# Optimization experiments

Hardware: AMD Instinct MI355X
Metric: run time of the kernel (lower is better)

## Reference

```python
import jax, jax.numpy as jnp
import numpy as np

HIDDEN = 256
HORIZON = 24
FMET = 16
OUT = 1
EPS = 1e-5


def setup_inputs() -> dict:
    key = jax.random.key(0)
    ks = jax.random.split(key, 12)
    B, N = 16, 1000
    final_h = jax.random.normal(ks[0], (B, N, HIDDEN), dtype=jnp.float32)
    future_met = jax.random.normal(ks[1], (B, HORIZON, N, FMET), dtype=jnp.float32)
    # step_queries: xavier_uniform over (max_horizon, hidden)
    lim_q = float(np.sqrt(6.0 / (HORIZON + HIDDEN)))
    step_queries = jax.random.uniform(ks[2], (HORIZON, HIDDEN), minval=-lim_q, maxval=lim_q, dtype=jnp.float32)
    # future_met_proj: Linear(FMET -> HIDDEN); store weight as (FMET, HIDDEN)
    lim_fm = float(np.sqrt(1.0 / FMET))
    W_fm = jax.random.uniform(ks[3], (FMET, HIDDEN), minval=-lim_fm, maxval=lim_fm, dtype=jnp.float32)
    b_fm = jax.random.uniform(ks[4], (HIDDEN,), minval=-lim_fm, maxval=lim_fm, dtype=jnp.float32)
    gamma = jnp.ones((HIDDEN,), dtype=jnp.float32)
    beta = jnp.zeros((HIDDEN,), dtype=jnp.float32)
    lim1 = float(np.sqrt(1.0 / HIDDEN))
    W1 = jax.random.uniform(ks[5], (HIDDEN, HIDDEN), minval=-lim1, maxval=lim1, dtype=jnp.float32)
    b1 = jax.random.uniform(ks[6], (HIDDEN,), minval=-lim1, maxval=lim1, dtype=jnp.float32)
    W2 = jax.random.uniform(ks[7], (HIDDEN, OUT), minval=-lim1, maxval=lim1, dtype=jnp.float32)
    b2 = jax.random.uniform(ks[8], (OUT,), minval=-lim1, maxval=lim1, dtype=jnp.float32)
    return {
        "final_h": final_h,
        "future_met": future_met,
        "step_queries": step_queries,
        "W_fm": W_fm,
        "b_fm": b_fm,
        "gamma": gamma,
        "beta": beta,
        "W1": W1,
        "b1": b1,
        "W2": W2,
        "b2": b2,
    }


def _layer_norm(x, gamma, beta):
    mu = jnp.mean(x, axis=-1, keepdims=True)
    var = jnp.mean(jnp.square(x - mu), axis=-1, keepdims=True)
    return (x - mu) * jax.lax.rsqrt(var + EPS) * gamma + beta


def reference(final_h, future_met, step_queries, W_fm, b_fm, gamma, beta, W1, b1, W2, b2):
    # final_h: (B, N, H); future_met: (B, T, N, F)
    # combined: (B, N, T, H) = broadcast(final_h) + queries + proj(future_met)
    combined = final_h[:, :, None, :] + step_queries[None, None, :, :]
    fm = jnp.transpose(future_met, (0, 2, 1, 3))  # (B, N, T, F)
    combined = combined + (jnp.einsum("bntf,fh->bnth", fm, W_fm) + b_fm)
    x = _layer_norm(combined, gamma, beta)
    x = jax.nn.gelu(x @ W1 + b1, approximate=False)
    # dropout is identity in eval mode
    out = x @ W2 + b2  # (B, N, T, OUT)
    return jnp.transpose(out, (0, 2, 1, 3))  # (B, T, N, OUT)
```

## Files before the change

kernel.cpp:

```cpp
#include <hip/hip_runtime.h>
#include <hip/hip_bf16.h>
#include <stdint.h>

#define MROWS 32
#define LDA   264
#define FMS   40

typedef __bf16 bf16x8 __attribute__((ext_vector_type(8)));
typedef float  f32x4  __attribute__((ext_vector_type(4)));
typedef float  f32x2  __attribute__((ext_vector_type(2)));

__device__ __forceinline__ unsigned short f2bf(float f) {
    union { float f; uint32_t u; } v; v.f = f;
    return (unsigned short)((v.u + 0x7FFFu + ((v.u >> 16) & 1u)) >> 16);
}

__device__ __forceinline__ ushort2 pk_bf16(float a, float b) {
    union { __hip_bfloat162 v; ushort2 u; } c;
    c.v = __float22bfloat162_rn(make_float2(a, b));
    return c.u;
}

template <int CTRL>
__device__ __forceinline__ float dpp_radd(float x) {
    union { float f; int i; } a, b;
    a.f = x;
    b.i = __builtin_amdgcn_update_dpp(0, a.i, CTRL, 0xF, 0xF, true);
    return x + b.f;
}
#define ROW_SHR1 0x111
#define ROW_SHR2 0x112
#define ROW_SHR4 0x114
#define ROW_SHR8 0x118
__device__ __forceinline__ float dpp_rowsum(float x) {
    x = dpp_radd<ROW_SHR1>(x);
    x = dpp_radd<ROW_SHR2>(x);
    x = dpp_radd<ROW_SHR4>(x);
    x = dpp_radd<ROW_SHR8>(x);
    return x;
}

__device__ __forceinline__ f32x2 gelu_fast2(f32x2 v) {
    const f32x2 t = v * v;
    f32x2 p = t * 0.044715f + 1.0f;
    const f32x2 u = v * p;
    f32x2 e;
    e.x = __builtin_amdgcn_exp2f(u.x * -2.3021131160186336f);
    e.y = __builtin_amdgcn_exp2f(u.y * -2.3021131160186336f);
    f32x2 r;
    r.x = __builtin_amdgcn_rcpf(1.0f + e.x);
    r.y = __builtin_amdgcn_rcpf(1.0f + e.y);
    return v * r;
}

__device__ __forceinline__ int frag_n(int f) {
    return (f & 0xC0) | ((f & 3) << 4) | ((f >> 2) & 15);
}

__global__ __launch_bounds__(256) void prep1(const float* __restrict__ W1,
                                             const float* __restrict__ step_q,
                                             const float* __restrict__ b_fm,
                                             const float* __restrict__ W_fm,
                                             const float* __restrict__ gamma,
                                             const float* __restrict__ beta,
                                             unsigned short* __restrict__ w1frag,
                                             float* __restrict__ sqb,
                                             unsigned short* __restrict__ wfmfrag,
                                             float* __restrict__ gpart,
                                             float* __restrict__ bpart) {
    const int blk = blockIdx.x, tid = threadIdx.x;
    if (blk < 8) {
        __shared__ unsigned short T[256][40];
        const int kk = blk;
        float sg = 0.f, sb = 0.f;
        #pragma unroll
        for (int r = 0; r < 32; ++r) {
            const int klog = frag_n((kk << 5) + r);
            const float wv = W1[klog * 256 + tid];
            const float gv = gamma[klog];
            sg = fmaf(gv, wv, sg);
            sb = fmaf(beta[klog], wv, sb);
            T[tid][r] = f2bf(wv * gv);
        }
        gpart[(kk << 8) + tid] = sg;
        bpart[(kk << 8) + tid] = sb;
        __syncthreads();
        #pragma unroll
        for (int f = 0; f < 4; ++f) {
            const int fi = (f << 8) + tid;
            const int l = fi & 63, j = (fi >> 6) & 3, w = fi >> 8;
            const int n = (w << 6) + (j << 4) + (l & 15);
            const uint4 v = *(const uint4*)&T[n][(l >> 4) << 3];
            *(uint4*)&w1frag[((w << 5) + (j << 3) + kk) * 512 + (l << 3)] = v;
        }
    } else if (blk < 32) {
        const int t = blk - 8;
        const int n = frag_n(tid);
        sqb[t * 256 + tid] = step_q[t * 256 + n] + b_fm[n];
    } else {
        const int f  = blk - 32;
        const int fr = (f << 8) + tid;
        const int l = fr & 63, j = (fr >> 6) & 3, w = fr >> 8;
        const int n = (w << 6) + (j << 4) + (l & 15);
        const int qr = l >> 4;
        #pragma unroll
        for (int e = 0; e < 8; ++e) {
            const int k = (qr << 3) + e;
            wfmfrag[(fr << 3) + e] = (k < 16) ? f2bf(W_fm[(k << 8) + n]) : (unsigned short)0;
        }
    }
}

__global__ __launch_bounds__(256) void prep2(const float* __restrict__ gpart,
                                             const float* __restrict__ bpart,
                                             const float* __restrict__ b1,
                                             const float* __restrict__ W2,
                                             float* __restrict__ gw1f,
                                             float* __restrict__ b1tf,
                                             float* __restrict__ w2f) {
    const int tid = threadIdx.x;
    const int n = frag_n(tid);
    float sg = 0.f, sb = 0.f;
    #pragma unroll
    for (int kk = 0; kk < 8; ++kk) {
        sg += gpart[(kk << 8) + n];
        sb += bpart[(kk << 8) + n];
    }
    gw1f[tid] = sg;
    b1tf[tid] = sb + b1[n];
    w2f[tid]  = W2[n];
}

__global__ __launch_bounds__(256, 6) void fused_head(
    const float* __restrict__ final_h, const float* __restrict__ future_met,
    const float* __restrict__ b2,      const unsigned short* __restrict__ w1frag,
    const float* __restrict__ sqb,     const unsigned short* __restrict__ wfmfrag,
    const float* __restrict__ gw1f,    const float* __restrict__ b1tf,
    const float* __restrict__ w2f,     float* __restrict__ out)
{
    __shared__ __align__(16) unsigned short Abuf[MROWS * LDA];
    __shared__ __align__(16) unsigned short fmA[MROWS * FMS];
    __shared__ float2 red[4][MROWS];
    __shared__ float2 mv[MROWS];
    __shared__ float  part[4][MROWS];

    const int tid = threadIdx.x;
    const int w   = tid >> 6;
    const int l   = tid & 63;
    const int col = l & 15;
    const int qr  = l >> 4;
    const int m0  = blockIdx.x * MROWS;
    const int bn0 = m0 / 24;
    const int tt0 = m0 - bn0 * 24;
    const int fb  = (w << 6) + (col << 2);

    if (tid < 128) {
        const int row = tid >> 2, f0 = (tid & 3) << 2;
        const int tta = tt0 + row;
        const int sub = (tta >= 24) + (tta >= 48);
        const int tt  = tta - sub * 24;
        const int bn  = bn0 + sub;
        const int b   = bn / 1000, n = bn - b * 1000;
        const float4 v = *(const float4*)&future_met[((((b * 24 + tt) * 1000) + n) << 4) + f0];
        ushort2 lo = pk_bf16(v.x, v.y), hi = pk_bf16(v.z, v.w);
        ushort4 o; o.x = lo.x; o.y = lo.y; o.z = hi.x; o.w = hi.y;
        *(ushort4*)&fmA[row * FMS + f0] = o;
    }
    {
        const int row = tid >> 3, k = 16 + ((tid & 7) << 1);
        *(unsigned int*)&fmA[row * FMS + k] = 0u;
    }
    __syncthreads();

    const int dlo = qr << 2;
    const int slo = ((tt0 + dlo) >= 24) + ((tt0 + dlo) >= 48);
    const int shi = ((tt0 + dlo + 19) >= 24) + ((tt0 + dlo + 19) >= 48);
    float flo[4], fhi[4];
    {
        const float* fhl = final_h + ((bn0 + slo) << 8) + (w << 6) + col;
        const float* fhh = final_h + ((bn0 + shi) << 8) + (w << 6) + col;
        #pragma unroll
        for (int j = 0; j < 4; ++j) { flo[j] = fhl[j << 4]; fhi[j] = fhh[j << 4]; }
    }

    f32x4 acc[2][4];
    #pragma unroll
    for (int i = 0; i < 2; ++i) {
        #pragma unroll
        for (int r = 0; r < 4; ++r) {
            const int d   = (i << 4) + (qr << 2) + r;
            const int tta = tt0 + d;
            const int sub = (tta >= 24) + (tta >= 48);
            const int tt  = tta - sub * 24;
            const bool lo = (sub == slo);
            const float4 sb4 = *(const float4*)&sqb[(tt << 8) + fb];
            acc[i][0][r] = (lo ? flo[0] : fhi[0]) + sb4.x;
            acc[i][1][r] = (lo ? flo[1] : fhi[1]) + sb4.y;
            acc[i][2][r] = (lo ? flo[2] : fhi[2]) + sb4.z;
            acc[i][3][r] = (lo ? flo[3] : fhi[3]) + sb4.w;
        }
    }
    {
        const bf16x8 af0 = *(const bf16x8*)&fmA[col * FMS + (qr << 3)];
        const bf16x8 af1 = *(const bf16x8*)&fmA[(16 + col) * FMS + (qr << 3)];
        const unsigned short* Bwf = wfmfrag + (w << 11) + (l << 3);
        #pragma unroll
        for (int j = 0; j < 4; ++j) {
            const bf16x8 bf = *(const bf16x8*)(Bwf + (j << 9));
            acc[0][j] = __builtin_amdgcn_mfma_f32_16x16x32_bf16(af0, bf, acc[0][j], 0, 0, 0);
            acc[1][j] = __builtin_amdgcn_mfma_f32_16x16x32_bf16(af1, bf, acc[1][j], 0, 0, 0);
        }
    }

    #pragma unroll
    for (int i = 0; i < 2; ++i) {
        #pragma unroll
        for (int r = 0; r < 4; ++r) {
            const int m = (i << 4) + (qr << 2) + r;
            const f32x2 vA = {acc[i][0][r], acc[i][1][r]};
            const f32x2 vB = {acc[i][2][r], acc[i][3][r]};
            const f32x2 sv = vA + vB;
            const f32x2 qv = vA * vA + vB * vB;
            float s = sv.x + sv.y;
            float q = qv.x + qv.y;
            const ushort2 p01 = pk_bf16(vA.x, vA.y);
            const ushort2 p23 = pk_bf16(vB.x, vB.y);
            s = dpp_rowsum(s);
            q = dpp_rowsum(q);
            if (col == 15) red[w][m] = make_float2(s, q);
            ushort4 o; o.x = p01.x; o.y = p01.y; o.z = p23.x; o.w = p23.y;
            *(ushort4*)&Abuf[m * LDA + (w << 6) + (col << 2)] = o;
        }
    }
    __syncthreads();

    if (tid < MROWS) {
        const float2 a0 = red[0][tid], a1 = red[1][tid], a2 = red[2][tid], a3 = red[3][tid];
        const float S = a0.x + a1.x + a2.x + a3.x;
        const float Q = a0.y + a1.y + a2.y + a3.y;
        const float mu = S * 0.00390625f;
        const float rstd = rsqrtf(Q * 0.00390625f - mu * mu + 1e-5f);
        mv[tid] = make_float2(mu, rstd);
    }

    #pragma unroll
    for (int i = 0; i < 2; ++i)
        #pragma unroll
        for (int j = 0; j < 4; ++j)
            acc[i][j] = (f32x4){0.f, 0.f, 0.f, 0.f};

    {
        const unsigned short* Bw  = w1frag + (w << 14) + (l << 3);
        const unsigned short* Ab0 = &Abuf[col * LDA + (qr << 3)];
        const unsigned short* Ab1 = &Abuf[(16 + col) * LDA + (qr << 3)];
        #pragma unroll
        for (int kk = 0; kk < 8; ++kk) {
            const bf16x8 a0 = *(const bf16x8*)(Ab0 + (kk << 5));
            const bf16x8 a1 = *(const bf16x8*)(Ab1 + (kk << 5));
            #pragma unroll
            for (int j = 0; j < 4; ++j) {
                const bf16x8 bf = *(const bf16x8*)(Bw + (j << 12) + (kk << 9));
                acc[0][j] = __builtin_amdgcn_mfma_f32_16x16x32_bf16(a0, bf, acc[0][j], 0, 0, 0);
                acc[1][j] = __builtin_amdgcn_mfma_f32_16x16x32_bf16(a1, bf, acc[1][j], 0, 0, 0);
            }
        }
    }

    const float4 gw4 = *(const float4*)&gw1f[fb];
    const float4 bt4 = *(const float4*)&b1tf[fb];
    const float4 w24 = *(const float4*)&w2f[fb];
    const f32x2 gwA = {gw4.x, gw4.y}, gwB = {gw4.z, gw4.w};
    const f32x2 btA = {bt4.x, bt4.y}, btB = {bt4.z, bt4.w};
    const f32x2 w2A = {w24.x, w24.y}, w2B = {w24.z, w24.w};
    __syncthreads();

    #pragma unroll
    for (int i = 0; i < 2; ++i) {
        #pragma unroll
        for (int r = 0; r < 4; ++r) {
            const int m = (i << 4) + (qr << 2) + r;
            const float2 p = mv[m];
            const float cm = -p.x * p.y;
            const f32x2 baseA = gwA * cm + btA;
            const f32x2 baseB = gwB * cm + btB;
            const f32x2 accA = {acc[i][0][r], acc[i][1][r]};
            const f32x2 accB = {acc[i][2][r], acc[i][3][r]};
            const f32x2 yA = accA * p.y + baseA;
            const f32x2 yB = accB * p.y + baseB;
            const f32x2 gvA = gelu_fast2(yA);
            const f32x2 gvB = gelu_fast2(yB);
            const f32x2 pp2 = gvA * w2A + gvB * w2B;
            float pp = pp2.x + pp2.y;
            pp = dpp_rowsum(pp);
            if (col == 15) part[w][m] = pp;
        }
    }
    __syncthreads();

    if (tid < MROWS) {
        const int m = m0 + tid;
        const float val = part[0][tid] + part[1][tid] + part[2][tid] + part[3][tid] + b2[0];
        const int bn = m / 24, tt = m - bn * 24;
        const int b  = bn / 1000, n = bn - b * 1000;
        out[(b * 24 + tt) * 1000 + n] = val;
    }
}

extern "C" void kernel_launch(void* const* d_in, const int* in_sizes, int n_in,
                              void* d_out, int out_size, void* d_ws, size_t ws_size,
                              hipStream_t stream) {
    const float* final_h    = (const float*)d_in[0];
    const float* future_met = (const float*)d_in[1];
    const float* step_q     = (const float*)d_in[2];
    const float* W_fm       = (const float*)d_in[3];
    const float* b_fm       = (const float*)d_in[4];
    const float* gamma      = (const float*)d_in[5];
    const float* beta       = (const float*)d_in[6];
    const float* W1         = (const float*)d_in[7];
    const float* b1         = (const float*)d_in[8];
    const float* W2         = (const float*)d_in[9];
    const float* b2         = (const float*)d_in[10];

    unsigned short* w1frag  = (unsigned short*)d_ws;
    float*          sqb     = (float*)((char*)d_ws + 131072);
    unsigned short* wfmfrag = (unsigned short*)((char*)d_ws + 155648);
    float*          gpart   = (float*)((char*)d_ws + 188416);
    float*          bpart   = (float*)((char*)d_ws + 196608);
    float*          gw1f    = (float*)((char*)d_ws + 204800);
    float*          b1tf    = (float*)((char*)d_ws + 205824);
    float*          w2f     = (float*)((char*)d_ws + 206848);
    float* out = (float*)d_out;

    prep1<<<36, 256, 0, stream>>>(W1, step_q, b_fm, W_fm, gamma, beta,
                                  w1frag, sqb, wfmfrag, gpart, bpart);
    prep2<<<1, 256, 0, stream>>>(gpart, bpart, b1, W2, gw1f, b1tf, w2f);
    fused_head<<<12000, 256, 0, stream>>>(final_h, future_met, b2,
                                          w1frag, sqb, wfmfrag, gw1f, b1tf, w2f, out);
}
```

Before: 199.4 us.

## Distribute W1 over the sum: precompute final_h@W1 per node, small per-step GEMMs

Uses linearity of the first matmul over the input sum (final_h + query + projected met). final_h·(γ∘W1) is computed once per (b,n) in a new prep kernel and stored to workspace. The step-query and met-projection terms are folded into W1 (a 16x256 fragment and a 24x256 table), so the main kernel runs one small K=32 MFMA instead of the full 256x256 GEMM per row. LayerNorm statistics still come from the un-normalized combined vector. This cuts main-kernel matmul work 24-fold at the cost of a 16MB fp32 intermediate write and read, plus a fallback path when workspace is too small.

```diff
diff --git a/kernel.cpp b/kernel.cpp
--- a/kernel.cpp
+++ b/kernel.cpp
@@ -67,10 +67,13 @@
                                              float* __restrict__ sqb,
                                              unsigned short* __restrict__ wfmfrag,
                                              float* __restrict__ gpart,
-                                             float* __restrict__ bpart) {
+                                             float* __restrict__ bpart,
+                                             float* __restrict__ WFWp,
+                                             float* __restrict__ SQWp) {
+    __shared__ unsigned short T[256][40];
+    __shared__ float redw[8][32][41];
     const int blk = blockIdx.x, tid = threadIdx.x;
     if (blk < 8) {
-        __shared__ unsigned short T[256][40];
         const int kk = blk;
         float sg = 0.f, sb = 0.f;
         #pragma unroll
@@ -97,7 +100,7 @@
         const int t = blk - 8;
         const int n = frag_n(tid);
         sqb[t * 256 + tid] = step_q[t * 256 + n] + b_fm[n];
-    } else {
+    } else if (blk < 36) {
         const int f  = blk - 32;
         const int fr = (f << 8) + tid;
         const int l = fr & 63, j = (fr >> 6) & 3, w = fr >> 8;
@@ -107,6 +110,40 @@
         for (int e = 0; e < 8; ++e) {
             const int k = (qr << 3) + e;
             wfmfrag[(fr << 3) + e] = (k < 16) ? f2bf(W_fm[(k << 8) + n]) : (unsigned short)0;
+        }
+    } else {
+        const int kc = tid >> 5, cl = tid & 31;
+        const int n  = ((blk - 36) << 5) + cl;
+        float wfw[16];
+        float sqw[24];
+        #pragma unroll
+        for (int f = 0; f < 16; ++f) wfw[f] = 0.f;
+        #pragma unroll
+        for (int t = 0; t < 24; ++t) sqw[t] = 0.f;
+        for (int hh = 0; hh < 32; ++hh) {
+            const int h = (kc << 5) + hh;
+            const float g1 = gamma[h] * W1[(h << 8) + n];
+            #pragma unroll
+            for (int f = 0; f < 16; ++f)
+                wfw[f] = fmaf(W_fm[(f << 8) + h], g1, wfw[f]);
+            const float bf = b_fm[h];
+            #pragma unroll
+            for (int t = 0; t < 24; ++t)
+                sqw[t] = fmaf(step_q[(t << 8) + h] + bf, g1, sqw[t]);
+        }
+        #pragma unroll
+        for (int f = 0; f < 16; ++f) redw[kc][cl][f] = wfw[f];
+        #pragma unroll
+        for (int t = 0; t < 24; ++t) redw[kc][cl][16 + t] = sqw[t];
+        __syncthreads();
+        for (int e = tid; e < 1280; e += 256) {
+            const int cl2 = e & 31, v = e >> 5;
+            float s = 0.f;
+            #pragma unroll
+            for (int k2 = 0; k2 < 8; ++k2) s += redw[k2][cl2][v];
+            const int nn = ((blk - 36) << 5) + cl2;
+            if (v < 16) WFWp[(v << 8) + nn] = s;
+            else        SQWp[((v - 16) << 8) + nn] = s;
         }
     }
 }
@@ -131,14 +168,111 @@
     w2f[tid]  = W2[n];
 }
 
+__global__ __launch_bounds__(256) void prep3(const float* __restrict__ final_h,
+                                             const unsigned short* __restrict__ w1frag,
+                                             const float* __restrict__ gpart,
+                                             const float* __restrict__ bpart,
+                                             const float* __restrict__ b1,
+                                             const float* __restrict__ W2,
+                                             const float* __restrict__ WFWp,
+                                             const float* __restrict__ SQWp,
+                                             float* __restrict__ gw1f,
+                                             float* __restrict__ b1tf,
+                                             float* __restrict__ w2f,
+                                             unsigned short* __restrict__ wfwfrag,
+                                             float* __restrict__ sqwf,
+                                             float* __restrict__ FHW) {
+    __shared__ __align__(16) unsigned short Abuf[MROWS * LDA];
+    const int blk = blockIdx.x, tid = threadIdx.x;
+    if (blk == 500) {
+        const int n = frag_n(tid);
+        float sg = 0.f, sb = 0.f;
+        #pragma unroll
+        for (int kk = 0; kk < 8; ++kk) {
+            sg += gpart[(kk << 8) + n];
+            sb += bpart[(kk << 8) + n];
+        }
+        gw1f[tid] = sg;
+        b1tf[tid] = sb + b1[n];
+        w2f[tid]  = W2[n];
+        #pragma unroll
+        for (int f = 0; f < 4; ++f) {
+            const int fr = (f << 8) + tid;
+            const int l = fr & 63, j = (fr >> 6) & 3, wq = fr >> 8;
+            const int nn = (wq << 6) + (j << 4) + (l & 15);
+            const int qr2 = l >> 4;
+            #pragma unroll
+            for (int e = 0; e < 8; ++e) {
+                const int k = (qr2 << 3) + e;
+                wfwfrag[(fr << 3) + e] = (k < 16) ? f2bf(WFWp[(k << 8) + nn]) : (unsigned short)0;
+            }
+        }
+        #pragma unroll
+        for (int t = 0; t < 24; ++t)
+            sqwf[(t << 8) + tid] = SQWp[(t << 8) + n];
+        return;
+    }
+    const int w = tid >> 6, l = tid & 63;
+    const int col = l & 15, qr = l >> 4;
+    const int fb = (w << 6) + (col << 2);
+    const int R0 = blk << 5;
+    #pragma unroll
+    for (int i = 0; i < 2; ++i) {
+        #pragma unroll
+        for (int r = 0; r < 4; ++r) {
+            const int m = (i << 4) + (qr << 2) + r;
+            const float* src = final_h + ((R0 + m) << 8) + (w << 6) + col;
+            const ushort2 p01 = pk_bf16(src[0],  src[16]);
+            const ushort2 p23 = pk_bf16(src[32], src[48]);
+            ushort4 o; o.x = p01.x; o.y = p01.y; o.z = p23.x; o.w = p23.y;
+            *(ushort4*)&Abuf[m * LDA + fb] = o;
+        }
+    }
+    __syncthreads();
+    f32x4 acc[2][4];
+    #pragma unroll
+    for (int i = 0; i < 2; ++i)
+        #pragma unroll
+        for (int j = 0; j < 4; ++j)
+            acc[i][j] = (f32x4){0.f, 0.f, 0.f, 0.f};
+    {
+        const unsigned short* Bw  = w1frag + (w << 14) + (l << 3);
+        const unsigned short* Ab0 = &Abuf[col * LDA + (qr << 3)];
+        const unsigned short* Ab1 = &Abuf[(16 + col) * LDA + (qr << 3)];
+        #pragma unroll
+        for (int kk = 0; kk < 8; ++kk) {
+            const bf16x8 a0 = *(const bf16x8*)(Ab0 + (kk << 5));
+            const bf16x8 a1 = *(const bf16x8*)(Ab1 + (kk << 5));
+            #pragma unroll
+            for (int j = 0; j < 4; ++j) {
+                const bf16x8 bf = *(const bf16x8*)(Bw + (j << 12) + (kk << 9));
+                acc[0][j] = __builtin_amdgcn_mfma_f32_16x16x32_bf16(a0, bf, acc[0][j], 0, 0, 0);
+                acc[1][j] = __builtin_amdgcn_mfma_f32_16x16x32_bf16(a1, bf, acc[1][j], 0, 0, 0);
+            }
+        }
+    }
+    #pragma unroll
+    for (int i = 0; i < 2; ++i) {
+        #pragma unroll
+        for (int r = 0; r < 4; ++r) {
+            const int m = (i << 4) + (qr << 2) + r;
+            float4 st;
+            st.x = acc[i][0][r]; st.y = acc[i][1][r];
+            st.z = acc[i][2][r]; st.w = acc[i][3][r];
+            *(float4*)&FHW[((R0 + m) << 8) + fb] = st;
+        }
+    }
+}
+
 __global__ __launch_bounds__(256, 6) void fused_head(
     const float* __restrict__ final_h, const float* __restrict__ future_met,
-    const float* __restrict__ b2,      const unsigned short* __restrict__ w1frag,
-    const float* __restrict__ sqb,     const unsigned short* __restrict__ wfmfrag,
+    const float* __restrict__ b2,      const float* __restrict__ sqb,
+    const unsigned short* __restrict__ wfmfrag,
     const float* __restrict__ gw1f,    const float* __restrict__ b1tf,
-    const float* __restrict__ w2f,     float* __restrict__ out)
+    const float* __restrict__ w2f,     const unsigned short* __restrict__ wfwfrag,
+    const float* __restrict__ sqwf,    const float* __restrict__ FHW,
+    float* __restrict__ out)
 {
-    __shared__ __align__(16) unsigned short Abuf[MROWS * LDA];
     __shared__ __align__(16) unsigned short fmA[MROWS * FMS];
     __shared__ float2 red[4][MROWS];
     __shared__ float2 mv[MROWS];
@@ -200,9 +334,9 @@
             acc[i][3][r] = (lo ? flo[3] : fhi[3]) + sb4.w;
         }
     }
-    {
-        const bf16x8 af0 = *(const bf16x8*)&fmA[col * FMS + (qr << 3)];
-        const bf16x8 af1 = *(const bf16x8*)&fmA[(16 + col) * FMS + (qr << 3)];
+    const bf16x8 af0 = *(const bf16x8*)&fmA[col * FMS + (qr << 3)];
+    const bf16x8 af1 = *(const bf16x8*)&fmA[(16 + col) * FMS + (qr << 3)];
+    {
         const unsigned short* Bwf = wfmfrag + (w << 11) + (l << 3);
         #pragma unroll
         for (int j = 0; j < 4; ++j) {
@@ -223,13 +357,9 @@
             const f32x2 qv = vA * vA + vB * vB;
             float s = sv.x + sv.y;
             float q = qv.x + qv.y;
-            const ushort2 p01 = pk_bf16(vA.x, vA.y);
-            const ushort2 p23 = pk_bf16(vB.x, vB.y);
             s = dpp_rowsum(s);
             q = dpp_rowsum(q);
             if (col == 15) red[w][m] = make_float2(s, q);
-            ushort4 o; o.x = p01.x; o.y = p01.y; o.z = p23.x; o.w = p23.y;
-            *(ushort4*)&Abuf[m * LDA + (w << 6) + (col << 2)] = o;
         }
     }
     __syncthreads();
@@ -244,25 +374,28 @@
     }
 
     #pragma unroll
-    for (int i = 0; i < 2; ++i)
-        #pragma unroll
-        for (int j = 0; j < 4; ++j)
-            acc[i][j] = (f32x4){0.f, 0.f, 0.f, 0.f};
-
-    {
-        const unsigned short* Bw  = w1frag + (w << 14) + (l << 3);
-        const unsigned short* Ab0 = &Abuf[col * LDA + (qr << 3)];
-        const unsigned short* Ab1 = &Abuf[(16 + col) * LDA + (qr << 3)];
-        #pragma unroll
-        for (int kk = 0; kk < 8; ++kk) {
-            const bf16x8 a0 = *(const bf16x8*)(Ab0 + (kk << 5));
-            const bf16x8 a1 = *(const bf16x8*)(Ab1 + (kk << 5));
-            #pragma unroll
-            for (int j = 0; j < 4; ++j) {
-                const bf16x8 bf = *(const bf16x8*)(Bw + (j << 12) + (kk << 9));
-                acc[0][j] = __builtin_amdgcn_mfma_f32_16x16x32_bf16(a0, bf, acc[0][j], 0, 0, 0);
-                acc[1][j] = __builtin_amdgcn_mfma_f32_16x16x32_bf16(a1, bf, acc[1][j], 0, 0, 0);
-            }
+    for (int i = 0; i < 2; ++i) {
+        #pragma unroll
+        for (int r = 0; r < 4; ++r) {
+            const int d   = (i << 4) + (qr << 2) + r;
+            const int tta = tt0 + d;
+            const int sub = (tta >= 24) + (tta >= 48);
+            const int tt  = tta - sub * 24;
+            const float4 fw = *(const float4*)&FHW[((bn0 + sub) << 8) + fb];
+            const float4 sw = *(const float4*)&sqwf[(tt << 8) + fb];
+            acc[i][0][r] = fw.x + sw.x;
+            acc[i][1][r] = fw.y + sw.y;
+            acc[i][2][r] = fw.z + sw.z;
+            acc[i][3][r] = fw.w + sw.w;
+        }
+    }
+    {
+        const unsigned short* Bw2 = wfwfrag + (w << 11) + (l << 3);
+        #pragma unroll
+        for (int j = 0; j < 4; ++j) {
+            const bf16x8 bfv = *(const bf16x8*)(Bw2 + (j << 9));
+            acc[0][j] = __builtin_amdgcn_mfma_f32_16x16x32_bf16(af0, bfv, acc[0][j], 0, 0, 0);
+            acc[1][j] = __builtin_amdgcn_mfma_f32_16x16x32_bf16(af1, bfv, acc[1][j], 0, 0, 0);
         }
     }
 
@@ -306,6 +439,181 @@
     }
 }
 
+__global__ __launch_bounds__(256, 6) void fused_head_v3(
+    const float* __restrict__ final_h, const float* __restrict__ future_met,
+    const float* __restrict__ b2,      const unsigned short* __restrict__ w1frag,
+    const float* __restrict__ sqb,     const unsigned short* __restrict__ wfmfrag,
+    const float* __restrict__ gw1f,    const float* __restrict__ b1tf,
+    const float* __restrict__ w2f,     float* __restrict__ out)
+{
+    __shared__ __align__(16) unsigned short Abuf[MROWS * LDA];
+    __shared__ __align__(16) unsigned short fmA[MROWS * FMS];
+    __shared__ float2 red[4][MROWS];
+    __shared__ float2 mv[MROWS];
+    __shared__ float  part[4][MROWS];
+
+    const int tid = threadIdx.x;
+    const int w   = tid >> 6;
+    const int l   = tid & 63;
+    const int col = l & 15;
+    const int qr  = l >> 4;
+    const int m0  = blockIdx.x * MROWS;
+    const int bn0 = m0 / 24;
+    const int tt0 = m0 - bn0 * 24;
+    const int fb  = (w << 6) + (col << 2);
+
+    if (tid < 128) {
+        const int row = tid >> 2, f0 = (tid & 3) << 2;
+        const int tta = tt0 + row;
+        const int sub = (tta >= 24) + (tta >= 48);
+        const int tt  = tta - sub * 24;
+        const int bn  = bn0 + sub;
+        const int b   = bn / 1000, n = bn - b * 1000;
+        const float4 v = *(const float4*)&future_met[((((b * 24 + tt) * 1000) + n) << 4) + f0];
+        ushort2 lo = pk_bf16(v.x, v.y), hi = pk_bf16(v.z, v.w);
+        ushort4 o; o.x = lo.x; o.y = lo.y; o.z = hi.x; o.w = hi.y;
+        *(ushort4*)&fmA[row * FMS + f0] = o;
+    }
+    {
+        const int row = tid >> 3, k = 16 + ((tid & 7) << 1);
+        *(unsigned int*)&fmA[row * FMS + k] = 0u;
+    }
+    __syncthreads();
+
+    const int dlo = qr << 2;
+    const int slo = ((tt0 + dlo) >= 24) + ((tt0 + dlo) >= 48);
+    const int shi = ((tt0 + dlo + 19) >= 24) + ((tt0 + dlo + 19) >= 48);
+    float flo[4], fhi[4];
+    {
+        const float* fhl = final_h + ((bn0 + slo) << 8) + (w << 6) + col;
+        const float* fhh = final_h + ((bn0 + shi) << 8) + (w << 6) + col;
+        #pragma unroll
+        for (int j = 0; j < 4; ++j) { flo[j] = fhl[j << 4]; fhi[j] = fhh[j << 4]; }
+    }
+
+    f32x4 acc[2][4];
+    #pragma unroll
+    for (int i = 0; i < 2; ++i) {
+        #pragma unroll
+        for (int r = 0; r < 4; ++r) {
+            const int d   = (i << 4) + (qr << 2) + r;
+            const int tta = tt0 + d;
+            const int sub = (tta >= 24) + (tta >= 48);
+            const int tt  = tta - sub * 24;
+            const bool lo = (sub == slo);
+            const float4 sb4 = *(const float4*)&sqb[(tt << 8) + fb];
+            acc[i][0][r] = (lo ? flo[0] : fhi[0]) + sb4.x;
+            acc[i][1][r] = (lo ? flo[1] : fhi[1]) + sb4.y;
+            acc[i][2][r] = (lo ? flo[2] : fhi[2]) + sb4.z;
+            acc[i][3][r] = (lo ? flo[3] : fhi[3]) + sb4.w;
+        }
+    }
+    {
+        const bf16x8 af0 = *(const bf16x8*)&fmA[col * FMS + (qr << 3)];
+        const bf16x8 af1 = *(const bf16x8*)&fmA[(16 + col) * FMS + (qr << 3)];
+        const unsigned short* Bwf = wfmfrag + (w << 11) + (l << 3);
+        #pragma unroll
+        for (int j = 0; j < 4; ++j) {
+            const bf16x8 bf = *(const bf16x8*)(Bwf + (j << 9));
+            acc[0][j] = __builtin_amdgcn_mfma_f32_16x16x32_bf16(af0, bf, acc[0][j], 0, 0, 0);
+            acc[1][j] = __builtin_amdgcn_mfma_f32_16x16x32_bf16(af1, bf, acc[1][j], 0, 0, 0);
+        }
+    }
+
+    #pragma unroll
+    for (int i = 0; i < 2; ++i) {
+        #pragma unroll
+        for (int r = 0; r < 4; ++r) {
+            const int m = (i << 4) + (qr << 2) + r;
+            const f32x2 vA = {acc[i][0][r], acc[i][1][r]};
+            const f32x2 vB = {acc[i][2][r], acc[i][3][r]};
+            const f32x2 sv = vA + vB;
+            const f32x2 qv = vA * vA + vB * vB;
+            float s = sv.x + sv.y;
+            float q = qv.x + qv.y;
+            const ushort2 p01 = pk_bf16(vA.x, vA.y);
+            const ushort2 p23 = pk_bf16(vB.x, vB.y);
+            s = dpp_rowsum(s);
+            q = dpp_rowsum(q);
+            if (col == 15) red[w][m] = make_float2(s, q);
+            ushort4 o; o.x = p01.x; o.y = p01.y; o.z = p23.x; o.w = p23.y;
+            *(ushort4*)&Abuf[m * LDA + (w << 6) + (col << 2)] = o;
+        }
+    }
+    __syncthreads();
+
+    if (tid < MROWS) {
+        const float2 a0 = red[0][tid], a1 = red[1][tid], a2 = red[2][tid], a3 = red[3][tid];
+        const float S = a0.x + a1.x + a2.x + a3.x;
+        const float Q = a0.y + a1.y + a2.y + a3.y;
+        const float mu = S * 0.00390625f;
+        const float rstd = rsqrtf(Q * 0.00390625f - mu * mu + 1e-5f);
+        mv[tid] = make_float2(mu, rstd);
+    }
+
+    #pragma unroll
+    for (int i = 0; i < 2; ++i)
+        #pragma unroll
+        for (int j = 0; j < 4; ++j)
+            acc[i][j] = (f32x4){0.f, 0.f, 0.f, 0.f};
+
+    {
+        const unsigned short* Bw  = w1frag + (w << 14) + (l << 3);
+        const unsigned short* Ab0 = &Abuf[col * LDA + (qr << 3)];
+        const unsigned short* Ab1 = &Abuf[(16 + col) * LDA + (qr << 3)];
+        #pragma unroll
+        for (int kk = 0; kk < 8; ++kk) {
+            const bf16x8 a0 = *(const bf16x8*)(Ab0 + (kk << 5));
+            const bf16x8 a1 = *(const bf16x8*)(Ab1 + (kk << 5));
+            #pragma unroll
+            for (int j = 0; j < 4; ++j) {
+                const bf16x8 bf = *(const bf16x8*)(Bw + (j << 12) + (kk << 9));
+                acc[0][j] = __builtin_amdgcn_mfma_f32_16x16x32_bf16(a0, bf, acc[0][j], 0, 0, 0);
+                acc[1][j] = __builtin_amdgcn_mfma_f32_16x16x32_bf16(a1, bf, acc[1][j], 0, 0, 0);
+            }
+        }
+    }
+
+    const float4 gw4 = *(const float4*)&gw1f[fb];
+    const float4 bt4 = *(const float4*)&b1tf[fb];
+    const float4 w24 = *(const float4*)&w2f[fb];
+    const f32x2 gwA = {gw4.x, gw4.y}, gwB = {gw4.z, gw4.w};
+    const f32x2 btA = {bt4.x, bt4.y}, btB = {bt4.z, bt4.w};
+    const f32x2 w2A = {w24.x, w24.y}, w2B = {w24.z, w24.w};
+    __syncthreads();
+
+    #pragma unroll
+    for (int i = 0; i < 2; ++i) {
+        #pragma unroll
+        for (int r = 0; r < 4; ++r) {
+            const int m = (i << 4) + (qr << 2) + r;
+            const float2 p = mv[m];
+            const float cm = -p.x * p.y;
+            const f32x2 baseA = gwA * cm + btA;
+            const f32x2 baseB = gwB * cm + btB;
+            const f32x2 accA = {acc[i][0][r], acc[i][1][r]};
+            const f32x2 accB = {acc[i][2][r], acc[i][3][r]};
+            const f32x2 yA = accA * p.y + baseA;
+            const f32x2 yB = accB * p.y + baseB;
+            const f32x2 gvA = gelu_fast2(yA);
+            const f32x2 gvB = gelu_fast2(yB);
+            const f32x2 pp2 = gvA * w2A + gvB * w2B;
+            float pp = pp2.x + pp2.y;
+            pp = dpp_rowsum(pp);
+            if (col == 15) part[w][m] = pp;
+        }
+    }
+    __syncthreads();
+
+    if (tid < MROWS) {
+        const int m = m0 + tid;
+        const float val = part[0][tid] + part[1][tid] + part[2][tid] + part[3][tid] + b2[0];
+        const int bn = m / 24, tt = m - bn * 24;
+        const int b  = bn / 1000, n = bn - b * 1000;
+        out[(b * 24 + tt) * 1000 + n] = val;
+    }
+}
+
 extern "C" void kernel_launch(void* const* d_in, const int* in_sizes, int n_in,
                               void* d_out, int out_size, void* d_ws, size_t ws_size,
                               hipStream_t stream) {
@@ -321,19 +629,36 @@
     const float* W2         = (const float*)d_in[9];
     const float* b2         = (const float*)d_in[10];
 
-    unsigned short* w1frag  = (unsigned short*)d_ws;
-    float*          sqb     = (float*)((char*)d_ws + 131072);
-    unsigned short* wfmfrag = (unsigned short*)((char*)d_ws + 155648);
-    float*          gpart   = (float*)((char*)d_ws + 188416);
-    float*          bpart   = (float*)((char*)d_ws + 196608);
-    float*          gw1f    = (float*)((char*)d_ws + 204800);
-    float*          b1tf    = (float*)((char*)d_ws + 205824);
-    float*          w2f     = (float*)((char*)d_ws + 206848);
+    char* ws = (char*)d_ws;
+    unsigned short* w1frag  = (unsigned short*)(ws);
+    float*          sqb     = (float*)(ws + 131072);
+    unsigned short* wfmfrag = (unsigned short*)(ws + 155648);
+    float*          gpart   = (float*)(ws + 172032);
+    float*          bpart   = (float*)(ws + 180224);
+    float*          gw1f    = (float*)(ws + 188416);
+    float*          b1tf    = (float*)(ws + 189440);
+    float*          w2f     = (float*)(ws + 190464);
+    float*          WFWp    = (float*)(ws + 191488);
+    float*          SQWp    = (float*)(ws + 207872);
+    unsigned short* wfwfrag = (unsigned short*)(ws + 232448);
+    float*          sqwf    = (float*)(ws + 248832);
+    float*          FHW     = (float*)(ws + 274432);
     float* out = (float*)d_out;
 
-    prep1<<<36, 256, 0, stream>>>(W1, step_q, b_fm, W_fm, gamma, beta,
-                                  w1frag, sqb, wfmfrag, gpart, bpart);
-    prep2<<<1, 256, 0, stream>>>(gpart, bpart, b1, W2, gw1f, b1tf, w2f);
-    fused_head<<<12000, 256, 0, stream>>>(final_h, future_met, b2,
-                                          w1frag, sqb, wfmfrag, gw1f, b1tf, w2f, out);
-}
+    const size_t WS_NEEDED = 274432u + 16384000u;
+    if (ws_size >= WS_NEEDED) {
+        prep1<<<44, 256, 0, stream>>>(W1, step_q, b_fm, W_fm, gamma, beta,
+                                      w1frag, sqb, wfmfrag, gpart, bpart, WFWp, SQWp);
+        prep3<<<501, 256, 0, stream>>>(final_h, w1frag, gpart, bpart, b1, W2,
+                                       WFWp, SQWp, gw1f, b1tf, w2f,
+                                       wfwfrag, sqwf, FHW);
+        fused_head<<<12000, 256, 0, stream>>>(final_h, future_met, b2, sqb, wfmfrag,
+                                              gw1f, b1tf, w2f, wfwfrag, sqwf, FHW, out);
+    } else {
+        prep1<<<36, 256, 0, stream>>>(W1, step_q, b_fm, W_fm, gamma, beta,
+                                      w1frag, sqb, wfmfrag, gpart, bpart, WFWp, SQWp);
+        prep2<<<1, 256, 0, stream>>>(gpart, bpart, b1, W2, gw1f, b1tf, w2f);
+        fused_head_v3<<<12000, 256, 0, stream>>>(final_h, future_met, b2, w1frag, sqb,
+                                                 wfmfrag, gw1f, b1tf, w2f, out);
+    }
+}
```

Result: slower. 225.3 us (+13.0%).
